# Optimization experiments

Hardware: AMD Instinct MI355X
Metric: run time of the kernel (lower is better)

The kernel has to match this reference:

```python
import jax, jax.numpy as jnp
import numpy as np

N_HARMONIC = 6
CONCAT = (3,)  # cfg.append_distance: concat embedding after this layer index
N_LAYERS = 8


def harmonic_embedding(x):
    # x: [N, 3] -> [N, 6*2*3 + 3] = [N, 39]
    freqs = 2.0 ** jnp.arange(N_HARMONIC, dtype=x.dtype)  # omega0 = 1.0, logspace
    embed = (x[..., None] * freqs).reshape(*x.shape[:-1], -1)  # [N, 18]
    return jnp.concatenate([jnp.sin(embed), jnp.cos(embed), x], axis=-1)


def setup_inputs() -> dict:
    key = jax.random.key(0)
    N, H, E = 262144, 256, 39
    ks = jax.random.split(key, 11)
    inp = {"points": jax.random.normal(ks[0], (N, 3), dtype=jnp.float32)}
    in_dims = [E, H, H, H, E + H, H, H, H]  # skip-concat before layer 4
    for i, d_in in enumerate(in_dims):
        scale = 1.0 / np.sqrt(d_in)
        inp[f"w{i}"] = jax.random.normal(ks[i + 1], (d_in, H), dtype=jnp.float32) * scale
        inp[f"b{i}"] = jnp.zeros((H,), dtype=jnp.float32)
    inp["wsdf"] = jax.random.normal(ks[9], (H, 1), dtype=jnp.float32) * (1.0 / np.sqrt(H))
    inp["bsdf"] = jnp.zeros((1,), dtype=jnp.float32)
    return inp


def reference(points, w0, b0, w1, b1, w2, b2, w3, b3, w4, b4, w5, b5, w6, b6, w7, b7, wsdf, bsdf):
    ws = [w0, w1, w2, w3, w4, w5, w6, w7]
    bs = [b0, b1, b2, b3, b4, b5, b6, b7]
    emb = harmonic_embedding(points.reshape(-1, 3))  # [N, 39]
    x = emb
    for i in range(N_LAYERS):
        x = jax.nn.relu(x @ ws[i] + bs[i])
        if i in CONCAT:
            x = jnp.concatenate([emb, x], axis=-1)  # torch.cat([add, xyz])
    return x @ wsdf + bsdf  # [N, 1] signed distance
```

## Files before the change

### kernel.cpp

```cpp
#include <hip/hip_runtime.h>
#include <hip/hip_fp16.h>

typedef _Float16 f16x8 __attribute__((ext_vector_type(8)));
typedef float f32x4 __attribute__((ext_vector_type(4)));

#define T 64
#define S 328

struct LayerPtrs {
  const float* w[8];
  const float* b[8];
};


__global__ void prep_weights(LayerPtrs P, f16x8* __restrict__ wf) {
  int gid = blockIdx.x * 256 + threadIdx.x;
  if (gid >= 61440) return;
  const int WOFF8[9] = {0,2048,10240,18432,26624,36864,45056,53248,61440};
  const int DIN[8]   = {39,256,256,256,295,256,256,256};
  int l = 0;
  while (gid >= WOFF8[l+1]) ++l;
  int f    = gid - WOFF8[l];
  int lane = f & 63;
  int t2   = f >> 6;
  int ntg  = t2 & 15;
  int kc   = t2 >> 4;
  int col  = (ntg << 4) + (lane & 15);
  int rbase = kc * 32 + ((lane >> 4) << 3);
  const float* w = P.w[l];
  f16x8 v;
#pragma unroll
  for (int j = 0; j < 8; ++j) {
    int r = rbase + j;
    float x = 0.f;
    if (l == 4) {
      if (r < 39)                 x = w[r * 256 + col];
      else if (r >= 40 && r < 296) x = w[(r - 1) * 256 + col];
    } else {
      if (r < DIN[l])             x = w[r * 256 + col];
    }
    v[j] = (_Float16)x;
  }
  wf[gid] = v;
}

__global__ __launch_bounds__(256, 3)
void mlp_fused(const float* __restrict__ points,
               LayerPtrs P,
               const f16x8* __restrict__ wf,
               const float* __restrict__ wsdf,
               const float* __restrict__ bsdf,
               float* __restrict__ out) {
  __shared__ __align__(16) _Float16 X[T * S];
  const int tid = threadIdx.x;
  const int blk = blockIdx.x;

  if (tid < T) {
    int p = blk * T + tid;
    float xyz[3] = {points[p*3+0], points[p*3+1], points[p*3+2]};
    _Float16* row = &X[tid * S];
#pragma unroll
    for (int c = 0; c < 3; ++c) {
      float fr = 1.f;
#pragma unroll
      for (int k = 0; k < 6; ++k) {
        float e = xyz[c] * fr;
        row[c*6 + k]      = (_Float16)sinf(e);
        row[18 + c*6 + k] = (_Float16)cosf(e);
        fr *= 2.f;
      }
      row[36 + c] = (_Float16)xyz[c];
    }
    for (int c = 39; c < 64; ++c)  row[c] = (_Float16)0.f;
    for (int c = 296; c < 320; ++c) row[c] = (_Float16)0.f;
  }
  __syncthreads();

  const int lane = tid & 63;
  const int wv   = tid >> 6;
  const int l16  = lane & 15;
  const int quad = lane >> 4;

  const int KP[8]    = {64,256,256,256,320,256,256,256};
  const int CO[8]    = {0,40,40,40,0,40,40,40};
  const int WOFF8[8] = {0,2048,10240,18432,26624,36864,45056,53248};

  for (int l = 0; l < 8; ++l) {
    const int nc = KP[l] >> 5;
    const int co = CO[l];
    const int wbase = WOFF8[l] + ((wv << 2) << 6) + lane;

    f32x4 acc[4][4];
#pragma unroll
    for (int mt = 0; mt < 4; ++mt)
#pragma unroll
      for (int nt = 0; nt < 4; ++nt)
        acc[mt][nt] = (f32x4){0.f, 0.f, 0.f, 0.f};

    for (int kc = 0; kc < nc; ++kc) {
      f16x8 bfr[4];
#pragma unroll
      for (int nt = 0; nt < 4; ++nt)
        bfr[nt] = wf[wbase + (kc << 10) + (nt << 6)];
      f16x8 afr[4];
#pragma unroll
      for (int mt = 0; mt < 4; ++mt)
        afr[mt] = *(const f16x8*)&X[(mt*16 + l16) * S + co + kc*32 + quad*8];
#pragma unroll
      for (int mt = 0; mt < 4; ++mt)
#pragma unroll
        for (int nt = 0; nt < 4; ++nt)
          acc[mt][nt] = __builtin_amdgcn_mfma_f32_16x16x32_f16(afr[mt], bfr[nt], acc[mt][nt], 0, 0, 0);
    }

    float bv[4];
    const float* bp = P.b[l];
#pragma unroll
    for (int nt = 0; nt < 4; ++nt)
      bv[nt] = bp[(wv << 6) + (nt << 4) + l16];

    __syncthreads();
#pragma unroll
    for (int mt = 0; mt < 4; ++mt)
#pragma unroll
      for (int nt = 0; nt < 4; ++nt)
#pragma unroll
        for (int r = 0; r < 4; ++r) {
          float v = acc[mt][nt][r] + bv[nt];
          v = fmaxf(v, 0.f);
          X[(mt*16 + quad*4 + r) * S + 40 + (wv << 6) + (nt << 4) + l16] = (_Float16)v;
        }
    __syncthreads();
  }

  {
    const int p = tid >> 2, part = tid & 3;
    float acc = 0.f;
    const _Float16* xr = &X[p * S + 40 + part * 64];
#pragma unroll
    for (int j = 0; j < 8; ++j) {
      f16x8 h = *(const f16x8*)&xr[j * 8];
#pragma unroll
      for (int e = 0; e < 8; ++e)
        acc += (float)h[e] * wsdf[part * 64 + j * 8 + e];
    }
    acc += __shfl_down(acc, 1);
    acc += __shfl_down(acc, 2);
    if (part == 0) out[blk * T + p] = acc + bsdf[0];
  }
}

extern "C" void kernel_launch(void* const* d_in, const int* in_sizes, int n_in,
                              void* d_out, int out_size, void* d_ws, size_t ws_size,
                              hipStream_t stream) {
  const float* points = (const float*)d_in[0];
  LayerPtrs P;
  for (int i = 0; i < 8; ++i) {
    P.w[i] = (const float*)d_in[1 + 2*i];
    P.b[i] = (const float*)d_in[2 + 2*i];
  }
  const float* wsdf = (const float*)d_in[17];
  const float* bsdf = (const float*)d_in[18];
  f16x8* wf = (f16x8*)d_ws;

  int N = in_sizes[0] / 3;
  prep_weights<<<240, 256, 0, stream>>>(P, wf);
  mlp_fused<<<N / T, 256, 0, stream>>>(points, P, wf, wsdf, bsdf, (float*)d_out);
}
```

Before: 359.4 us.

## Switch fused MLP to 32x32x16 MFMA with separate embedding buffer and unrolled layers

Rewrites the fused MLP main loop to use 32x32x16 f16 MFMA tiles, with weights as the A operand and points as B. The embedding now lives in its own shared buffer so the skip concat reads it directly, which cuts layer 0 and 4 padding from 32-wide to 16-wide K chunks. Layers are fully unrolled with compile-time K, bias loads and activation stores are vectorized, and launch bounds rise to four blocks per CU. The point is fewer MFMA issues and LDS reads per FLOP and less padded work, at the cost of higher register pressure from full unrolling and 4x16-float accumulators.

```diff
diff --git a/kernel.cpp b/kernel.cpp
--- a/kernel.cpp
+++ b/kernel.cpp
@@ -2,151 +2,200 @@
 #include <hip/hip_fp16.h>
 
 typedef _Float16 f16x8 __attribute__((ext_vector_type(8)));
-typedef float f32x4 __attribute__((ext_vector_type(4)));
-
-#define T 64
-#define S 328
+typedef _Float16 f16x4 __attribute__((ext_vector_type(4)));
+typedef float    f32x16 __attribute__((ext_vector_type(16)));
+typedef float    f32x4 __attribute__((ext_vector_type(4)));
+
+#define SH 264
+#define SE 56
 
 struct LayerPtrs {
   const float* w[8];
   const float* b[8];
 };
 
-
 __global__ void prep_weights(LayerPtrs P, f16x8* __restrict__ wf) {
   int gid = blockIdx.x * 256 + threadIdx.x;
-  if (gid >= 61440) return;
-  const int WOFF8[9] = {0,2048,10240,18432,26624,36864,45056,53248,61440};
-  const int DIN[8]   = {39,256,256,256,295,256,256,256};
+  if (gid >= 60416) return;
+  const int OFF[9] = {0,1536,9728,17920,26112,35840,44032,52224,60416};
   int l = 0;
-  while (gid >= WOFF8[l+1]) ++l;
-  int f    = gid - WOFF8[l];
+  while (gid >= OFF[l+1]) ++l;
+  int f = gid - OFF[l];
   int lane = f & 63;
-  int t2   = f >> 6;
-  int ntg  = t2 & 15;
-  int kc   = t2 >> 4;
-  int col  = (ntg << 4) + (lane & 15);
-  int rbase = kc * 32 + ((lane >> 4) << 3);
+  int t = f >> 6;
+  int mtile = t & 7;
+  int kc = t >> 3;
+  int col = mtile * 32 + (lane & 31);
+  int kb  = (lane >> 5) * 8;
   const float* w = P.w[l];
   f16x8 v;
 #pragma unroll
   for (int j = 0; j < 8; ++j) {
-    int r = rbase + j;
     float x = 0.f;
     if (l == 4) {
-      if (r < 39)                 x = w[r * 256 + col];
-      else if (r >= 40 && r < 296) x = w[(r - 1) * 256 + col];
+      if (kc < 3) {
+        int k = kc * 16 + kb + j;
+        if (k < 39) x = w[k * 256 + col];
+      } else {
+        int k = (kc - 3) * 16 + kb + j;
+        x = w[(39 + k) * 256 + col];
+      }
+    } else if (l == 0) {
+      int k = kc * 16 + kb + j;
+      if (k < 39) x = w[k * 256 + col];
     } else {
-      if (r < DIN[l])             x = w[r * 256 + col];
+      int k = kc * 16 + kb + j;
+      x = w[k * 256 + col];
     }
     v[j] = (_Float16)x;
   }
   wf[gid] = v;
 }
 
-__global__ __launch_bounds__(256, 3)
+template<int NKC>
+__device__ __forceinline__ void mm(const f16x8* __restrict__ wb,
+                                   const _Float16* __restrict__ b0,
+                                   const _Float16* __restrict__ b1,
+                                   f32x16 acc[2][2]) {
+#pragma unroll
+  for (int kc = 0; kc < NKC; ++kc) {
+    f16x8 a0 = wb[(kc * 8 + 0) * 64];
+    f16x8 a1 = wb[(kc * 8 + 1) * 64];
+    f16x8 v0 = *(const f16x8*)(b0 + kc * 16);
+    f16x8 v1 = *(const f16x8*)(b1 + kc * 16);
+    acc[0][0] = __builtin_amdgcn_mfma_f32_32x32x16_f16(a0, v0, acc[0][0], 0, 0, 0);
+    acc[0][1] = __builtin_amdgcn_mfma_f32_32x32x16_f16(a0, v1, acc[0][1], 0, 0, 0);
+    acc[1][0] = __builtin_amdgcn_mfma_f32_32x32x16_f16(a1, v0, acc[1][0], 0, 0, 0);
+    acc[1][1] = __builtin_amdgcn_mfma_f32_32x32x16_f16(a1, v1, acc[1][1], 0, 0, 0);
+  }
+}
+
+__device__ __forceinline__ void zero_acc(f32x16 acc[2][2]) {
+#pragma unroll
+  for (int mt = 0; mt < 2; ++mt)
+#pragma unroll
+    for (int nt = 0; nt < 2; ++nt)
+#pragma unroll
+      for (int r = 0; r < 16; ++r) acc[mt][nt][r] = 0.f;
+}
+
+__device__ __forceinline__ void store_act(f32x16 acc[2][2], const float* __restrict__ bp,
+                                          int wv, int lane, _Float16* __restrict__ H) {
+  int p0 = lane & 31, h = lane >> 5;
+#pragma unroll
+  for (int mt = 0; mt < 2; ++mt) {
+    int hb = wv * 64 + mt * 32 + 4 * h;
+#pragma unroll
+    for (int g = 0; g < 4; ++g) {
+      f32x4 bv = *(const f32x4*)&bp[hb + 8 * g];
+#pragma unroll
+      for (int nt = 0; nt < 2; ++nt) {
+        f16x4 o;
+#pragma unroll
+        for (int r = 0; r < 4; ++r) {
+          float x = acc[mt][nt][4 * g + r] + bv[r];
+          o[r] = (_Float16)fmaxf(x, 0.f);
+        }
+        *(f16x4*)&H[(nt * 32 + p0) * SH + hb + 8 * g] = o;
+      }
+    }
+  }
+}
+
+__global__ __launch_bounds__(256, 4)
 void mlp_fused(const float* __restrict__ points,
                LayerPtrs P,
                const f16x8* __restrict__ wf,
                const float* __restrict__ wsdf,
                const float* __restrict__ bsdf,
                float* __restrict__ out) {
-  __shared__ __align__(16) _Float16 X[T * S];
+  __shared__ __align__(16) _Float16 H[64 * SH];
+  __shared__ __align__(16) _Float16 E[64 * SE];
   const int tid = threadIdx.x;
   const int blk = blockIdx.x;
 
-  if (tid < T) {
-    int p = blk * T + tid;
-    float xyz[3] = {points[p*3+0], points[p*3+1], points[p*3+2]};
-    _Float16* row = &X[tid * S];
+  if (tid < 64) {
+    int p = blk * 64 + tid;
+    float xyz[3] = {points[p * 3 + 0], points[p * 3 + 1], points[p * 3 + 2]};
+    _Float16* row = &E[tid * SE];
 #pragma unroll
     for (int c = 0; c < 3; ++c) {
       float fr = 1.f;
 #pragma unroll
       for (int k = 0; k < 6; ++k) {
         float e = xyz[c] * fr;
-        row[c*6 + k]      = (_Float16)sinf(e);
-        row[18 + c*6 + k] = (_Float16)cosf(e);
+        row[c * 6 + k]      = (_Float16)sinf(e);
+        row[18 + c * 6 + k] = (_Float16)cosf(e);
         fr *= 2.f;
       }
       row[36 + c] = (_Float16)xyz[c];
     }
-    for (int c = 39; c < 64; ++c)  row[c] = (_Float16)0.f;
-    for (int c = 296; c < 320; ++c) row[c] = (_Float16)0.f;
+    for (int c = 39; c < SE; ++c) row[c] = (_Float16)0.f;
   }
   __syncthreads();
 
   const int lane = tid & 63;
   const int wv   = tid >> 6;
-  const int l16  = lane & 15;
-  const int quad = lane >> 4;
-
-  const int KP[8]    = {64,256,256,256,320,256,256,256};
-  const int CO[8]    = {0,40,40,40,0,40,40,40};
-  const int WOFF8[8] = {0,2048,10240,18432,26624,36864,45056,53248};
-
-  for (int l = 0; l < 8; ++l) {
-    const int nc = KP[l] >> 5;
-    const int co = CO[l];
-    const int wbase = WOFF8[l] + ((wv << 2) << 6) + lane;
-
-    f32x4 acc[4][4];
-#pragma unroll
-    for (int mt = 0; mt < 4; ++mt)
-#pragma unroll
-      for (int nt = 0; nt < 4; ++nt)
-        acc[mt][nt] = (f32x4){0.f, 0.f, 0.f, 0.f};
-
-    for (int kc = 0; kc < nc; ++kc) {
-      f16x8 bfr[4];
-#pragma unroll
-      for (int nt = 0; nt < 4; ++nt)
-        bfr[nt] = wf[wbase + (kc << 10) + (nt << 6)];
-      f16x8 afr[4];
-#pragma unroll
-      for (int mt = 0; mt < 4; ++mt)
-        afr[mt] = *(const f16x8*)&X[(mt*16 + l16) * S + co + kc*32 + quad*8];
-#pragma unroll
-      for (int mt = 0; mt < 4; ++mt)
-#pragma unroll
-        for (int nt = 0; nt < 4; ++nt)
-          acc[mt][nt] = __builtin_amdgcn_mfma_f32_16x16x32_f16(afr[mt], bfr[nt], acc[mt][nt], 0, 0, 0);
-    }
-
-    float bv[4];
-    const float* bp = P.b[l];
-#pragma unroll
-    for (int nt = 0; nt < 4; ++nt)
-      bv[nt] = bp[(wv << 6) + (nt << 4) + l16];
-
-    __syncthreads();
-#pragma unroll
-    for (int mt = 0; mt < 4; ++mt)
-#pragma unroll
-      for (int nt = 0; nt < 4; ++nt)
-#pragma unroll
-        for (int r = 0; r < 4; ++r) {
-          float v = acc[mt][nt][r] + bv[nt];
-          v = fmaxf(v, 0.f);
-          X[(mt*16 + quad*4 + r) * S + 40 + (wv << 6) + (nt << 4) + l16] = (_Float16)v;
-        }
+  const int p0   = lane & 31;
+  const int h    = lane >> 5;
+
+  const _Float16* e0 = &E[p0 * SE + h * 8];
+  const _Float16* e1 = &E[(32 + p0) * SE + h * 8];
+  const _Float16* h0 = &H[p0 * SH + h * 8];
+  const _Float16* h1 = &H[(32 + p0) * SH + h * 8];
+  const f16x8* wb = wf + wv * 128 + lane;
+
+  const int WOFF[8] = {0,1536,9728,17920,26112,35840,44032,52224};
+
+  f32x16 acc[2][2];
+
+  zero_acc(acc);
+  mm<3>(wb + WOFF[0], e0, e1, acc);
+  store_act(acc, P.b[0], wv, lane, H);
+  __syncthreads();
+
+#pragma unroll
+  for (int l = 1; l < 4; ++l) {
+    zero_acc(acc);
+    mm<16>(wb + WOFF[l], h0, h1, acc);
+    __syncthreads();
+    store_act(acc, P.b[l], wv, lane, H);
+    __syncthreads();
+  }
+
+  zero_acc(acc);
+  mm<3>(wb + WOFF[4], e0, e1, acc);
+  mm<16>(wb + WOFF[4] + 3 * 512, h0, h1, acc);
+  __syncthreads();
+  store_act(acc, P.b[4], wv, lane, H);
+  __syncthreads();
+
+#pragma unroll
+  for (int l = 5; l < 8; ++l) {
+    zero_acc(acc);
+    mm<16>(wb + WOFF[l], h0, h1, acc);
+    __syncthreads();
+    store_act(acc, P.b[l], wv, lane, H);
     __syncthreads();
   }
 
   {
     const int p = tid >> 2, part = tid & 3;
-    float acc = 0.f;
-    const _Float16* xr = &X[p * S + 40 + part * 64];
+    float a = 0.f;
+    const _Float16* xr = &H[p * SH + part * 64];
 #pragma unroll
     for (int j = 0; j < 8; ++j) {
-      f16x8 h = *(const f16x8*)&xr[j * 8];
-#pragma unroll
-      for (int e = 0; e < 8; ++e)
-        acc += (float)h[e] * wsdf[part * 64 + j * 8 + e];
-    }
-    acc += __shfl_down(acc, 1);
-    acc += __shfl_down(acc, 2);
-    if (part == 0) out[blk * T + p] = acc + bsdf[0];
+      f16x8 hh = *(const f16x8*)&xr[j * 8];
+      f32x4 wa = *(const f32x4*)&wsdf[part * 64 + j * 8];
+      f32x4 wc = *(const f32x4*)&wsdf[part * 64 + j * 8 + 4];
+      a += (float)hh[0] * wa[0] + (float)hh[1] * wa[1]
+         + (float)hh[2] * wa[2] + (float)hh[3] * wa[3]
+         + (float)hh[4] * wc[0] + (float)hh[5] * wc[1]
+         + (float)hh[6] * wc[2] + (float)hh[7] * wc[3];
+    }
+    a += __shfl_down(a, 1);
+    a += __shfl_down(a, 2);
+    if (part == 0) out[blk * 64 + p] = a + bsdf[0];
   }
 }
 
@@ -156,14 +205,14 @@
   const float* points = (const float*)d_in[0];
   LayerPtrs P;
   for (int i = 0; i < 8; ++i) {
-    P.w[i] = (const float*)d_in[1 + 2*i];
-    P.b[i] = (const float*)d_in[2 + 2*i];
+    P.w[i] = (const float*)d_in[1 + 2 * i];
+    P.b[i] = (const float*)d_in[2 + 2 * i];
   }
   const float* wsdf = (const float*)d_in[17];
   const float* bsdf = (const float*)d_in[18];
   f16x8* wf = (f16x8*)d_ws;
 
   int N = in_sizes[0] / 3;
-  prep_weights<<<240, 256, 0, stream>>>(P, wf);
-  mlp_fused<<<N / T, 256, 0, stream>>>(points, P, wf, wsdf, bsdf, (float*)d_out);
-}
+  prep_weights<<<236, 256, 0, stream>>>(P, wf);
+  mlp_fused<<<N / 64, 256, 0, stream>>>(points, P, wf, wsdf, bsdf, (float*)d_out);
+}
```

New measurement: 354.3 us. No clear change (-1.4%).
